# Kernel optimization log

Hardware: AMD Instinct MI355X
Metric: run time of the kernel (lower is better)

The kernel has to match this reference:

```python
import jax, jax.numpy as jnp
import numpy as np

BATCH = 32768
INPUT_DIM = 256
N_NEURONS = 128
MAX_DEGREE = 7  # D; features per input dim = D+1 = 8


def _cheb_features(x, degree):
    """Chebyshev T_0..T_degree of x [B, In] -> [B, In, degree+1] via recurrence.

    Matches torch.special.chebyshev_polynomial_t(x, n=d) for d = 0..degree.
    """
    T = [jnp.ones_like(x), x]
    for _ in range(2, degree + 1):
        T.append(2.0 * x * T[-1] - T[-2])
    return jnp.stack(T[: degree + 1], axis=-1)


def setup_inputs() -> dict:
    key = jax.random.key(0)
    k1, k2 = jax.random.split(key)
    # inputs in [0,1) keep Chebyshev values bounded, as in a normalized pipeline
    x = jax.random.uniform(k1, (BATCH, INPUT_DIM), dtype=jnp.float32)
    # per-neuron coefficient vectors over the dim-major [In*(D+1)] feature layout
    coeffs = jax.random.normal(k2, (N_NEURONS, INPUT_DIM * (MAX_DEGREE + 1)), dtype=jnp.float32) * 0.02
    return {"x": x, "coeffs": coeffs}


def reference(x, coeffs):
    B, In = x.shape
    D = coeffs.shape[1] // In - 1
    # [B, In, D+1] -> dim-major flatten matches torch.cat over per-dim stacks
    X = _cheb_features(x, D).reshape(B, In * (D + 1))
    # per-neuron dot products, then sum over neurons (KANLayer stack().sum(0))
    per_neuron = jnp.einsum("bf,nf->bn", X, coeffs)  # [B, n_neurons]
    return per_neuron.sum(axis=1, keepdims=True)  # [B, 1]
```

## Files before the change

### kernel.cpp

```cpp
#include <hip/hip_runtime.h>

#define BATCH     32768
#define IN_DIM    256
#define N_NEURONS 128
#define DEG1      8
#define FEAT      (IN_DIM * DEG1)
#define RS        (FEAT / 4)
#define XR4       (IN_DIM / 4)
#define NBLK      256
#define NTHR      512
#define RPW       16
#define XB        4


__global__ __launch_bounds__(NTHR, 2) void kan_fused(const float* __restrict__ x,
                                                     const float* __restrict__ coeffs,
                                                     float* __restrict__ out) {
    __shared__ float csum[FEAT];
    const int t    = threadIdx.x;
    const int lane = t & 63;
    const int wave = t >> 6;
    const int row0 = (blockIdx.x * (NTHR / 64) + wave) * RPW;

    const float4* xr = (const float4*)x + (size_t)row0 * XR4 + lane;

    float4 xa[XB], xb[XB];
#pragma unroll
    for (int r = 0; r < XB; ++r) xa[r] = xr[(size_t)r * XR4];

    const float4* cp = (const float4*)coeffs + t;
    float4 s1[16];
#pragma unroll
    for (int g = 0; g < 16; ++g) {
        const float4* pa = cp + (size_t)(4 * g) * RS;
        const float4* pb = cp + (size_t)(4 * (g + 16)) * RS;
        float4 a0 = pa[0], a1 = pa[RS], a2 = pa[2 * RS], a3 = pa[3 * RS];
        float4 b0 = pb[0], b1 = pb[RS], b2 = pb[2 * RS], b3 = pb[3 * RS];
        float4 s;
        s.x = (((a0.x + a1.x) + a2.x) + a3.x) + (((b0.x + b1.x) + b2.x) + b3.x);
        s.y = (((a0.y + a1.y) + a2.y) + a3.y) + (((b0.y + b1.y) + b2.y) + b3.y);
        s.z = (((a0.z + a1.z) + a2.z) + a3.z) + (((b0.z + b1.z) + b2.z) + b3.z);
        s.w = (((a0.w + a1.w) + a2.w) + a3.w) + (((b0.w + b1.w) + b2.w) + b3.w);
        s1[g] = s;
    }
#pragma unroll
    for (int stride = 8; stride >= 1; stride >>= 1) {
#pragma unroll
        for (int g = 0; g < 8; ++g) {
            if (g < stride) {
                s1[g].x += s1[g + stride].x;
                s1[g].y += s1[g + stride].y;
                s1[g].z += s1[g + stride].z;
                s1[g].w += s1[g + stride].w;
            }
        }
    }
    ((float4*)csum)[t] = s1[0];
    __syncthreads();

    float c[4][8];
    const float4* c4 = (const float4*)csum + (size_t)lane * 8;
#pragma unroll
    for (int j = 0; j < 4; ++j) {
        float4 a = c4[j * 2];
        float4 b = c4[j * 2 + 1];
        c[j][0] = a.x; c[j][1] = a.y; c[j][2] = a.z; c[j][3] = a.w;
        c[j][4] = b.x; c[j][5] = b.y; c[j][6] = b.z; c[j][7] = b.w;
    }

#pragma unroll
    for (int b = 0; b < RPW / XB; ++b) {
        if (b < RPW / XB - 1) {
#pragma unroll
            for (int r = 0; r < XB; ++r)
                xb[r] = xr[(size_t)((b + 1) * XB + r) * XR4];
        }
        float s[XB];
#pragma unroll
        for (int k = 0; k < XB; ++k) {
            float xs[4] = {xa[k].x, xa[k].y, xa[k].z, xa[k].w};
            float a = 0.f;
#pragma unroll
            for (int j = 0; j < 4; ++j) {
                const float xx = xs[j];
                const float two_x = xx + xx;
                a = fmaf(c[j][1], xx, a + c[j][0]);
                float tp = 1.f, tc = xx;
#pragma unroll
                for (int d = 2; d < 8; ++d) {
                    float tn = fmaf(two_x, tc, -tp);
                    a = fmaf(c[j][d], tn, a);
                    tp = tc; tc = tn;
                }
            }
#pragma unroll
            for (int off = 32; off > 0; off >>= 1) a += __shfl_down(a, off, 64);
            s[k] = a;
        }
        if (lane == 0)
            ((float4*)out)[row0 / 4 + b] = make_float4(s[0], s[1], s[2], s[3]);
#pragma unroll
        for (int r = 0; r < XB; ++r) xa[r] = xb[r];
    }
}

extern "C" void kernel_launch(void* const* d_in, const int* in_sizes, int n_in,
                              void* d_out, int out_size, void* d_ws, size_t ws_size,
                              hipStream_t stream) {
    const float* x      = (const float*)d_in[0];
    const float* coeffs = (const float*)d_in[1];
    float* out = (float*)d_out;
    (void)d_ws; (void)ws_size;

    kan_fused<<<NBLK, NTHR, 0, stream>>>(x, coeffs, out);
}
```

Measured before the change: 94.86 us.

## Double block size, halve rows per wave, split coeff reduction across thread halves

Moves to 1024-thread blocks with 8 rows per wave, keeping 256 blocks. The coefficient neuron-sum is split between the two 512-thread halves, each summing 8 of the 16 groups, and combined through a shared-memory bridge with an extra barrier. This is meant to shorten the per-block coefficient preamble and give the batch loop more waves. The shared csum array is padded (one float4 per 8) to reduce bank conflicts on the per-lane reads. The risk is extra synchronisation, and each block still redoes the full coefficient reduction.

Result: faster. 83.03 us (-12.5%).

```diff
diff --git a/kernel.cpp b/kernel.cpp
--- a/kernel.cpp
+++ b/kernel.cpp
@@ -8,62 +8,70 @@
 #define RS        (FEAT / 4)
 #define XR4       (IN_DIM / 4)
 #define NBLK      256
-#define NTHR      512
-#define RPW       16
+#define NTHR      1024
+#define WPB       (NTHR / 64)
+#define RPW       8
 #define XB        4
 
 
-__global__ __launch_bounds__(NTHR, 2) void kan_fused(const float* __restrict__ x,
+__global__ __launch_bounds__(NTHR, 4) void kan_fused(const float* __restrict__ x,
                                                      const float* __restrict__ coeffs,
                                                      float* __restrict__ out) {
-    __shared__ float csum[FEAT];
+    __shared__ float4 csum4[576];
+    __shared__ float4 bridge[512];
     const int t    = threadIdx.x;
     const int lane = t & 63;
     const int wave = t >> 6;
-    const int row0 = (blockIdx.x * (NTHR / 64) + wave) * RPW;
-
-    const float4* xr = (const float4*)x + (size_t)row0 * XR4 + lane;
+    const int row0 = (blockIdx.x * WPB + wave) * RPW;
 
     float4 xa[XB], xb[XB];
+    const float4* xr = (const float4*)x + (size_t)row0 * XR4 + lane;
 #pragma unroll
     for (int r = 0; r < XB; ++r) xa[r] = xr[(size_t)r * XR4];
 
-    const float4* cp = (const float4*)coeffs + t;
-    float4 s1[16];
+    {
+        const int col = t & 511;
+        const int odd = t >> 9;
+        const float4* cp = (const float4*)coeffs + col;
+        float4 s1[8];
 #pragma unroll
-    for (int g = 0; g < 16; ++g) {
-        const float4* pa = cp + (size_t)(4 * g) * RS;
-        const float4* pb = cp + (size_t)(4 * (g + 16)) * RS;
-        float4 a0 = pa[0], a1 = pa[RS], a2 = pa[2 * RS], a3 = pa[3 * RS];
-        float4 b0 = pb[0], b1 = pb[RS], b2 = pb[2 * RS], b3 = pb[3 * RS];
-        float4 s;
-        s.x = (((a0.x + a1.x) + a2.x) + a3.x) + (((b0.x + b1.x) + b2.x) + b3.x);
-        s.y = (((a0.y + a1.y) + a2.y) + a3.y) + (((b0.y + b1.y) + b2.y) + b3.y);
-        s.z = (((a0.z + a1.z) + a2.z) + a3.z) + (((b0.z + b1.z) + b2.z) + b3.z);
-        s.w = (((a0.w + a1.w) + a2.w) + a3.w) + (((b0.w + b1.w) + b2.w) + b3.w);
-        s1[g] = s;
+        for (int i = 0; i < 8; ++i) {
+            const int g = 2 * i + odd;
+            const float4* pa = cp + (size_t)(4 * g) * RS;
+            const float4* pb = cp + (size_t)(4 * (g + 16)) * RS;
+            float4 a0 = pa[0], a1 = pa[RS], a2 = pa[2 * RS], a3 = pa[3 * RS];
+            float4 b0 = pb[0], b1 = pb[RS], b2 = pb[2 * RS], b3 = pb[3 * RS];
+            s1[i].x = (((a0.x + a1.x) + a2.x) + a3.x) + (((b0.x + b1.x) + b2.x) + b3.x);
+            s1[i].y = (((a0.y + a1.y) + a2.y) + a3.y) + (((b0.y + b1.y) + b2.y) + b3.y);
+            s1[i].z = (((a0.z + a1.z) + a2.z) + a3.z) + (((b0.z + b1.z) + b2.z) + b3.z);
+            s1[i].w = (((a0.w + a1.w) + a2.w) + a3.w) + (((b0.w + b1.w) + b2.w) + b3.w);
+        }
+#pragma unroll
+        for (int i = 0; i < 4; ++i) {
+            s1[i].x += s1[i + 4].x; s1[i].y += s1[i + 4].y;
+            s1[i].z += s1[i + 4].z; s1[i].w += s1[i + 4].w;
+        }
+        s1[0].x += s1[2].x; s1[0].y += s1[2].y; s1[0].z += s1[2].z; s1[0].w += s1[2].w;
+        s1[1].x += s1[3].x; s1[1].y += s1[3].y; s1[1].z += s1[3].z; s1[1].w += s1[3].w;
+        s1[0].x += s1[1].x; s1[0].y += s1[1].y; s1[0].z += s1[1].z; s1[0].w += s1[1].w;
+
+        if (odd) bridge[col] = s1[0];
+        __syncthreads();
+        if (!odd) {
+            float4 wb = bridge[col];
+            float4 r;
+            r.x = s1[0].x + wb.x; r.y = s1[0].y + wb.y;
+            r.z = s1[0].z + wb.z; r.w = s1[0].w + wb.w;
+            csum4[col + (col >> 3)] = r;
+        }
+        __syncthreads();
     }
-#pragma unroll
-    for (int stride = 8; stride >= 1; stride >>= 1) {
-#pragma unroll
-        for (int g = 0; g < 8; ++g) {
-            if (g < stride) {
-                s1[g].x += s1[g + stride].x;
-                s1[g].y += s1[g + stride].y;
-                s1[g].z += s1[g + stride].z;
-                s1[g].w += s1[g + stride].w;
-            }
-        }
-    }
-    ((float4*)csum)[t] = s1[0];
-    __syncthreads();
 
     float c[4][8];
-    const float4* c4 = (const float4*)csum + (size_t)lane * 8;
 #pragma unroll
     for (int j = 0; j < 4; ++j) {
-        float4 a = c4[j * 2];
-        float4 b = c4[j * 2 + 1];
+        float4 a = csum4[lane * 9 + j * 2];
+        float4 b = csum4[lane * 9 + j * 2 + 1];
         c[j][0] = a.x; c[j][1] = a.y; c[j][2] = a.z; c[j][3] = a.w;
         c[j][4] = b.x; c[j][5] = b.y; c[j][6] = b.z; c[j][7] = b.w;
     }
```
